# Kernel optimization log

Measured on AMD Instinct MI355X. Metric: run time of the kernel, lower is better.

The kernel has to match this reference:

```python
import jax, jax.numpy as jnp
import numpy as np

BN_EPS = 1e-3  # keras BatchNormalization default epsilon


def _conv(x, w):
    # x: [B,H,W,Cin], w: [kh,kw,Cin,Cout], stride 1, SAME padding
    return jax.lax.conv_general_dilated(
        x, w, window_strides=(1, 1), padding='SAME',
        dimension_numbers=('NHWC', 'HWIO', 'NHWC'))


def _bn(x, g, b, m, v):
    return (x - m) * jax.lax.rsqrt(v + BN_EPS) * g + b


def _pam(x, wq, bq, wk, bk, wv, bv, gamma):
    # Position attention: softmax over HW x HW similarity of 1x1-conv q/k.
    B, H, W, C = x.shape
    q = (_conv(x, wq) + bq).reshape(B, H * W, -1)   # [B,HW,C/8]
    k = (_conv(x, wk) + bk).reshape(B, H * W, -1)   # [B,HW,C/8]
    v = (_conv(x, wv) + bv).reshape(B, H * W, C)    # [B,HW,C]
    energy = jnp.einsum('bic,bjc->bij', q, k)       # [B,HW,HW]
    att = jax.nn.softmax(energy, axis=-1)
    out = jnp.einsum('bij,bjc->bic', att, v).reshape(B, H, W, C)
    return gamma * out + x


def _cam(x, gamma):
    # Channel attention with max-subtract stabilization, softmax over C.
    B, H, W, C = x.shape
    X = x.reshape(B, H * W, C)                      # channel-last flat
    energy = jnp.einsum('bnc,bnd->bcd', X, X)       # [B,C,C]
    energy_new = jnp.max(energy, axis=-1, keepdims=True) - energy
    att = jax.nn.softmax(energy_new, axis=-1)       # [B,C,C]
    out = jnp.einsum('bcd,bnd->bnc', att, X).reshape(B, H, W, C)
    return gamma * out + x


def setup_inputs() -> dict:
    key = jax.random.key(0)
    ks = jax.random.split(key, 16)
    B, H, W = 4, 64, 64
    Cin, Ci, Cq, Cout = 512, 128, 16, 19
    s = 0.05
    d = {
        'x': jax.random.normal(ks[0], (B, H, W, Cin), jnp.float32),
        'w5a': jax.random.normal(ks[1], (3, 3, Cin, Ci), jnp.float32) * s,
        'w5c': jax.random.normal(ks[2], (3, 3, Cin, Ci), jnp.float32) * s,
        'wq': jax.random.normal(ks[3], (1, 1, Ci, Cq), jnp.float32) * s,
        'bq': jnp.zeros((Cq,), jnp.float32),
        'wk': jax.random.normal(ks[4], (1, 1, Ci, Cq), jnp.float32) * s,
        'bk': jnp.zeros((Cq,), jnp.float32),
        'wv': jax.random.normal(ks[5], (1, 1, Ci, Ci), jnp.float32) * s,
        'bv': jnp.zeros((Ci,), jnp.float32),
        'pam_gamma': jnp.float32(0.5),
        'cam_gamma': jnp.float32(0.5),
        'w51': jax.random.normal(ks[6], (3, 3, Ci, Ci), jnp.float32) * s,
        'w52': jax.random.normal(ks[7], (3, 3, Ci, Ci), jnp.float32) * s,
        'w8': jax.random.normal(ks[8], (1, 1, Ci, Cout), jnp.float32) * s,
    }
    for i, nm in enumerate(['bn1', 'bn2', 'bn3', 'bn4']):
        d[nm + '_g'] = jnp.ones((Ci,), jnp.float32)
        d[nm + '_b'] = jnp.zeros((Ci,), jnp.float32)
        d[nm + '_m'] = jax.random.normal(ks[9 + i], (Ci,), jnp.float32) * 0.1
        d[nm + '_v'] = jnp.ones((Ci,), jnp.float32)
    return d


def reference(x, w5a, w5c, wq, bq, wk, bk, wv, bv, pam_gamma, cam_gamma,
              w51, w52, w8,
              bn1_g, bn1_b, bn1_m, bn1_v,
              bn2_g, bn2_b, bn2_m, bn2_v,
              bn3_g, bn3_b, bn3_m, bn3_v,
              bn4_g, bn4_b, bn4_m, bn4_v):
    # PAM branch
    feat1 = jax.nn.relu(_bn(_conv(x, w5a), bn1_g, bn1_b, bn1_m, bn1_v))
    sa_feat = _pam(feat1, wq, bq, wk, bk, wv, bv, pam_gamma)
    sa_conv = jax.nn.relu(_bn(_conv(sa_feat, w51), bn3_g, bn3_b, bn3_m, bn3_v))
    # CAM branch
    feat2 = jax.nn.relu(_bn(_conv(x, w5c), bn2_g, bn2_b, bn2_m, bn2_v))
    sc_feat = _cam(feat2, cam_gamma)
    sc_conv = jax.nn.relu(_bn(_conv(sc_feat, w52), bn4_g, bn4_b, bn4_m, bn4_v))
    # Fused output (dropout is identity at inference)
    feat_sum = sa_conv + sc_conv
    return _conv(feat_sum, w8)
```

## Files before the change

kernel.cpp:

```cpp
#include <hip/hip_runtime.h>
#include <hip/hip_bf16.h>
#include <math.h>

#define BN_EPS 1e-3f
#define LOG2E 1.44269504088896f

constexpr int Bn = 4, Hn = 64, Wn = 64, CIN = 512, CI = 128;
constexpr int HWn = Hn * Wn;
constexpr int NPIX = Bn * HWn;
constexpr int COn = 19;

struct F8 { float4 lo, hi; };

__device__ __forceinline__ F8 f8zero() {
    F8 r; r.lo = make_float4(0.f,0.f,0.f,0.f); r.hi = make_float4(0.f,0.f,0.f,0.f); return r;
}
__device__ __forceinline__ void fma8(F8 &acc, float a, const float4 &wlo, const float4 &whi) {
    acc.lo.x = fmaf(a, wlo.x, acc.lo.x);
    acc.lo.y = fmaf(a, wlo.y, acc.lo.y);
    acc.lo.z = fmaf(a, wlo.z, acc.lo.z);
    acc.lo.w = fmaf(a, wlo.w, acc.lo.w);
    acc.hi.x = fmaf(a, whi.x, acc.hi.x);
    acc.hi.y = fmaf(a, whi.y, acc.hi.y);
    acc.hi.z = fmaf(a, whi.z, acc.hi.z);
    acc.hi.w = fmaf(a, whi.w, acc.hi.w);
}

typedef __attribute__((ext_vector_type(8)))  short    short8;
typedef __attribute__((ext_vector_type(8)))  _Float16 half8;
typedef __attribute__((ext_vector_type(16))) float    f32x16;

__device__ __forceinline__ f32x16 f16z() {
    f32x16 z;
    #pragma unroll
    for (int i = 0; i < 16; ++i) z[i] = 0.f;
    return z;
}
__device__ __forceinline__ unsigned f2b(float f) {
    union { float f; unsigned u; } c; c.f = f;
    return (c.u + 0x7FFFu + ((c.u >> 16) & 1u)) >> 16;
}
__device__ __forceinline__ unsigned pack2(float lo, float hi) {
    return (f2b(hi) << 16) | f2b(lo);
}
__device__ __forceinline__ unsigned pkb2(float a, float b) {
    __hip_bfloat16 ha = __float2bfloat16(a);
    __hip_bfloat16 hb = __float2bfloat16(b);
    return ((unsigned)*(unsigned short*)&hb << 16) | *(unsigned short*)&ha;
}
__device__ __forceinline__ void split2(float a, float b, unsigned &hi, unsigned &lo) {
    const unsigned ha = f2b(a), hb = f2b(b);
    union { unsigned u; float f; } ua, ub; ua.u = ha << 16; ub.u = hb << 16;
    hi = (hb << 16) | ha;
    lo = pack2(a - ua.f, b - ub.f);
}
__device__ __forceinline__ unsigned pkh2(float a, float b) {
    union { _Float16 h; unsigned short u; } ca, cb;
    ca.h = (_Float16)a; cb.h = (_Float16)b;
    return ((unsigned)cb.u << 16) | ca.u;
}

__global__ __launch_bounds__(256)
void k_prep_w(const float* __restrict__ w5a, const float* __restrict__ w5c,
              const float* __restrict__ w51, const float* __restrict__ w52,
              char* __restrict__ wt1F, char* __restrict__ wt2aF, char* __restrict__ wt2bF)
{
    int idx = blockIdx.x * 256 + threadIdx.x;
    if (idx < 589824) {
        const int jp = idx & 7, co = (idx >> 3) & 255, ct = idx >> 11;
        const int tap = ct % 9, c = ct / 9;
        const float* src = (co < 128) ? w5a : w5c;
        const int coc = co & 127;
        const int ci = c*16 + jp*2;
        const float a = src[((size_t)tap*CIN + ci)*CI + coc];
        const float b = src[((size_t)tap*CIN + ci + 1)*CI + coc];
        const int L = co*32 + jp*4;
        *(unsigned*)(wt1F + (size_t)ct*8192 + L) = pkh2(a, b);
    } else {
        int k = idx - 589824;
        if (k >= 147456) return;
        const float* src = (k < 73728) ? w51 : w52;
        char* dstF = (k < 73728) ? wt2aF : wt2bF;
        if (k >= 73728) k -= 73728;
        const int jp = k & 7, co = (k >> 3) & 127, ct = k >> 10;
        const int tap = ct % 9, c = ct / 9;
        const int ci = c*16 + jp*2;
        const float a = src[((size_t)tap*CI + ci)*CI + co];
        const float b = src[((size_t)tap*CI + ci + 1)*CI + co];
        const int L = co*32 + jp*4;
        *(unsigned*)(dstF + (size_t)ct*4096 + L) = pkh2(a, b);
    }
}

__global__ __launch_bounds__(256)
void k_prep_bn(const float* g1, const float* b1, const float* m1, const float* v1,
               const float* g2, const float* b2, const float* m2, const float* v2,
               const float* g3, const float* b3, const float* m3, const float* v3,
               const float* g4, const float* b4, const float* m4, const float* v4,
               float* bnAs, float* bnAb, float* bnBs, float* bnBb)
{
    const int t = threadIdx.x, c = t & 127;
    {
        const float *g = (t < 128) ? g1 : g2, *b = (t < 128) ? b1 : b2;
        const float *m = (t < 128) ? m1 : m2, *v = (t < 128) ? v1 : v2;
        const float s = g[c] * rsqrtf(v[c] + BN_EPS);
        bnAs[t] = s; bnAb[t] = b[c] - m[c]*s;
    }
    {
        const float *g = (t < 128) ? g3 : g4, *b = (t < 128) ? b3 : b4;
        const float *m = (t < 128) ? m3 : m4, *v = (t < 128) ? v3 : v4;
        const float s = g[c] * rsqrtf(v[c] + BN_EPS);
        bnBs[t] = s; bnBb[t] = b[c] - m[c]*s;
    }
}

__global__ __launch_bounds__(256)
void k_prep_x(const float* __restrict__ x, _Float16* __restrict__ xcv)
{
    __shared__ float Xl[16*520];
    const int t = threadIdx.x;
    const int pb = blockIdx.x * 16;
    #pragma unroll
    for (int i = 0; i < 8; ++i) {
        const int u = t + i*256;
        const int px = u >> 7, c4 = (u & 127) * 4;
        *(float4*)&Xl[px*520 + c4] = *(const float4*)&x[(size_t)(pb + px)*CIN + c4];
    }
    __syncthreads();
    const int rowg = pb >> 6, pixb = pb & 63;
    #pragma unroll
    for (int i = 0; i < 8; ++i) {
        const int u = t + i*256;
        const int chunk = u >> 6, rem = u & 63;
        const int pl = rem >> 2, u4 = rem & 3;
        const float* src = &Xl[pl*520 + chunk*16 + u4*4];
        uint2 v;
        v.x = pkh2(src[0], src[1]);
        v.y = pkh2(src[2], src[3]);
        *(uint2*)&xcv[(((size_t)rowg*32 + chunk)*64 + (pixb + pl))*16 + u4*4] = v;
    }
}

template<int NCHNK, int NCOTOT, int WCOBASE>
__global__ __launch_bounds__(256)
void k_convh(const _Float16* __restrict__ xcv0, const _Float16* __restrict__ xcv1,
             const _Float16* __restrict__ wtF0, const _Float16* __restrict__ wtF1,
             const float* __restrict__ bnS, const float* __restrict__ bnBi,
             float* __restrict__ out0, float* __restrict__ out1)
{
    constexpr int XPAGE = 66*32;
    constexpr int XCH   = 3*XPAGE;
    __shared__ __align__(16) char Xs[2*2*XCH];

    const int t    = threadIdx.x;
    const int wgid = blockIdx.x;
    const int xcd  = wgid & 7;
    const int sel  = xcd >> 2;
    const int ch2  = (xcd >> 1) & 1;
    const int row  = ((wgid >> 3) << 1) | (xcd & 1);
    const _Float16* xcv = sel ? xcv1 : xcv0;
    const _Float16* wtF = sel ? wtF1 : wtF0;
    float* dst = sel ? out1 : out0;

    const int hh = row & 63;
    const int dyLo = (hh == 0)  ? 1 : 0;
    const int dyHi = (hh == 63) ? 1 : 2;
    const int l = t & 63, w = t >> 6;
    const int lo5 = l & 31, hf = l >> 5;
    const int mi = w >> 1, nt = w & 1;
    const int corow = WCOBASE*sel + ch2*64 + nt*32 + lo5;

    bool sAct[7], sIn[7]; int sLoff[7]; unsigned sGoff[7];
    #pragma unroll
    for (int i = 0; i < 7; ++i) {
        const int u = t + i*256;
        sAct[i] = false; sIn[i] = false; sLoff[i] = 0; sGoff[i] = 0;
        if (u < 1584) {
            const int cc = (u >= 792) ? 1 : 0;
            const int uu = u - cc*792;
            const int dyr = uu/264, rs = uu - dyr*264;
            const int s = rs >> 2, u4 = rs & 3;
            sAct[i]  = (dyr >= dyLo && dyr <= dyHi);
            sIn[i]   = (s >= 1 && s <= 64);
            sLoff[i] = cc*XCH + dyr*XPAGE + ((s*32 + u4*8) ^ ((s & 7) << 4));
            sGoff[i] = (unsigned)(((row + dyr - 1)*NCHNK + cc)*1024 + (s - 1)*16 + u4*4);
        }
    }
    int xoff[3];
    #pragma unroll
    for (int dx = 0; dx < 3; ++dx) {
        const int s = mi*32 + lo5 + dx;
        xoff[dx] = (s*32 + hf*16) ^ ((s & 7) << 4);
    }

    f32x16 acc = f16z();
    half8 wA[9], wB[9];

    auto issueW9 = [&](int c, half8 (&wr)[9]) {
        #pragma unroll
        for (int tap = 0; tap < 9; ++tap)
            wr[tap] = *(const half8*)&wtF[((size_t)(c*9 + tap)*NCOTOT + corow)*16 + hf*8];
    };
    auto compC = [&](const char* Xb, int cc, const half8 (&wr)[9]) {
        #pragma unroll
        for (int dy = 0; dy < 3; ++dy) {
            if (dy < dyLo || dy > dyHi) continue;
            const char* Xp = Xb + cc*XCH + dy*XPAGE;
            #pragma unroll
            for (int dx = 0; dx < 3; ++dx) {
                const half8 xf = *(const half8*)(Xp + xoff[dx]);
                acc = __builtin_amdgcn_mfma_f32_32x32x16_f16(wr[dy*3 + dx], xf, acc, 0, 0, 0);
            }
        }
    };

    uint2 xr[7];
    auto loadX = [&](int cbase) {
        #pragma unroll
        for (int i = 0; i < 7; ++i) {
            uint2 v; v.x = 0u; v.y = 0u;
            if (sAct[i] && sIn[i])
                v = *(const uint2*)&xcv[(size_t)sGoff[i] + (size_t)cbase*1024];
            xr[i] = v;
        }
    };

    loadX(0);
    int p = 0;
    for (int c = 0; c < NCHNK; c += 2) {
        issueW9(c, wA);
        char* Xb = Xs + p*2*XCH;
        #pragma unroll
        for (int i = 0; i < 7; ++i)
            if (sAct[i]) *(uint2*)(Xb + sLoff[i]) = xr[i];
        __syncthreads();
        if (c + 2 < NCHNK) loadX(c + 2);
        issueW9(c + 1, wB);
        compC(Xb, 0, wA);
        compC(Xb, 1, wB);
        p ^= 1;
    }
    const int px = mi*32 + lo5;
    const size_t pg = (size_t)row*Wn + px;
    #pragma unroll
    for (int r = 0; r < 16; ++r) {
        const int crow = (r & 3) + 8*(r >> 2) + 4*hf;
        const int och = ch2*64 + nt*32 + crow;
        const int bnidx = sel*128 + och;
        dst[pg*CI + och] = fmaxf(fmaf(acc[r], bnS[bnidx], bnBi[bnidx]), 0.f);
    }
}

__global__ __launch_bounds__(256)
void k_qk(const float* __restrict__ feat1,
          const float* __restrict__ wq, const float* __restrict__ bq,
          const float* __restrict__ wk, const float* __restrict__ bk,
          __hip_bfloat16* __restrict__ qb, __hip_bfloat16* __restrict__ kb)
{
    __shared__ float Al[64*129];
    __shared__ __align__(16) float Wl[128*32];
    const int t = threadIdx.x;
    const int pb = blockIdx.x * 64;
    for (int idx = t; idx < 64*128; idx += 256) {
        const int p = idx >> 7, ci = idx & 127;
        Al[p*129 + ci] = feat1[(size_t)(pb + p)*CI + ci];
    }
    for (int idx = t; idx < 128*32; idx += 256) {
        const int ci = idx >> 5, c = idx & 31;
        Wl[idx] = (c < 16) ? wq[ci*16 + c] : wk[ci*16 + (c - 16)];
    }
    __syncthreads();
    const int p = t & 63, cg = t >> 6, co = cg * 8;
    F8 acc = f8zero();
    #pragma unroll 8
    for (int ci = 0; ci < 128; ++ci) {
        const float a = Al[p*129 + ci];
        const float4 wlo = *(const float4*)&Wl[ci*32 + co];
        const float4 whi = *(const float4*)&Wl[ci*32 + co + 4];
        fma8(acc, a, wlo, whi);
    }
    const float* af = (const float*)&acc;
    #pragma unroll
    for (int j = 0; j < 8; ++j) {
        const int c = co + j;
        if (c < 16) qb[(size_t)(pb + p)*16 + c]        = __float2bfloat16((af[j] + bq[c]) * LOG2E);
        else        kb[(size_t)(pb + p)*16 + (c - 16)] = __float2bfloat16(af[j] + bk[c - 16]);
    }
}

__global__ __launch_bounds__(256)
void k_v(const float* __restrict__ feat1, const float* __restrict__ wv,
         const float* __restrict__ bv, __hip_bfloat16* __restrict__ vbT)
{
    __shared__ float Al[32*129];
    __shared__ __align__(16) float Wl[64*128];
    const int t = threadIdx.x;
    const int pb = blockIdx.x * 32;
    for (int idx = t; idx < 32*128; idx += 256) {
        const int p = idx >> 7, ci = idx & 127;
        Al[p*129 + ci] = feat1[(size_t)(pb + p)*CI + ci];
    }
    const int px = t & 15, co = (t >> 4) * 8;
    F8 acc0 = f8zero(), acc1 = f8zero();
    for (int ch = 0; ch < 2; ++ch) {
        __syncthreads();
        #pragma unroll
        for (int r = 0; r < 8; ++r) {
            const int i4 = t + r*256;
            const int kk = i4 >> 5, c4 = (i4 & 31) * 4;
            *(float4*)&Wl[kk*128 + c4] = *(const float4*)&wv[(size_t)(ch*64 + kk)*CI + c4];
        }
        __syncthreads();
        #pragma unroll 4
        for (int kk = 0; kk < 64; ++kk) {
            const float a0 = Al[px*129 + ch*64 + kk];
            const float a1 = Al[(px+16)*129 + ch*64 + kk];
            const float4 wlo = *(const float4*)&Wl[kk*128 + co];
            const float4 whi = *(const float4*)&Wl[kk*128 + co + 4];
            fma8(acc0, a0, wlo, whi);
            fma8(acc1, a1, wlo, whi);
        }
    }
    const int p0 = pb + px;
    const int bb = p0 / HWn, pin0 = p0 % HWn;
    const int k16a = pin0 >> 4, ko = pin0 & 15;
    const float* a0f = (const float*)&acc0;
    const float* a1f = (const float*)&acc1;
    #pragma unroll
    for (int j = 0; j < 8; ++j) {
        const int c = co + j;
        const size_t base = ((size_t)bb*256*CI*16) + (size_t)c*16 + ko;
        vbT[base + (size_t)k16a*CI*16]       = __float2bfloat16(a0f[j] + bv[c]);
        vbT[base + (size_t)(k16a + 1)*CI*16] = __float2bfloat16(a1f[j] + bv[c]);
    }
}

__global__ __launch_bounds__(256)
void k_pam(const __hip_bfloat16* __restrict__ qb, const __hip_bfloat16* __restrict__ kb,
           const __hip_bfloat16* __restrict__ vbT, const float* __restrict__ feat1,
           const float* __restrict__ gamma, _Float16* __restrict__ saf_h)
{
    __shared__ __align__(16) char pbuf[16896];
    __shared__ float msArr[4][32];
    __shared__ float ssArr[4][32];
    __shared__ float ssum[32];
    const int t  = threadIdx.x;
    const int wv = t >> 6, l = t & 63;
    const int lo5 = l & 31, h = l >> 5;
    unsigned* Ppk = (unsigned*)(pbuf + wv*4096);
    float* osum = (float*)pbuf;

    const int q0 = blockIdx.x * 32;
    const int bb = q0 / HWn;
    const size_t jb = (size_t)bb * HWn;
    const __hip_bfloat16* vbB = vbT + (size_t)bb * 256 * CI * 16;

    const short8 qfrag = *(const short8*)&qb[(size_t)(q0 + lo5)*16 + 8*h];
    const f32x16 zro = f16z();

    f32x16 o[4];
    #pragma unroll
    for (int cb = 0; cb < 4; ++cb) o[cb] = f16z();

    float m_run = -1e30f, s_run = 0.f;

    for (int k0 = wv*1024; k0 < wv*1024 + 1024; k0 += 64) {
        const short8 kf0 = *(const short8*)&kb[(jb + k0 +      lo5)*16 + 8*h];
        const short8 kf1 = *(const short8*)&kb[(jb + k0 + 32 + lo5)*16 + 8*h];
        short8 vf[4][4];
        #pragma unroll
        for (int s = 0; s < 4; ++s)
            #pragma unroll
            for (int cb = 0; cb < 4; ++cb)
                vf[s][cb] = *(const short8*)&vbB[
                    (((size_t)(k0 >> 4) + s)*CI + cb*32 + lo5)*16 + 8*h];

        f32x16 e0 = __builtin_amdgcn_mfma_f32_32x32x16_bf16(kf0, qfrag, zro, 0, 0, 0);
        f32x16 e1 = __builtin_amdgcn_mfma_f32_32x32x16_bf16(kf1, qfrag, zro, 0, 0, 0);

        float mt = fmaxf(e0[0], e1[0]);
        #pragma unroll
        for (int r = 1; r < 16; ++r) mt = fmaxf(mt, fmaxf(e0[r], e1[r]));
        mt = fmaxf(mt, __shfl_xor(mt, 32));

        if (__any(mt > m_run + 11.5416f)) {
            const float mnew = fmaxf(m_run, mt);
            const float sc = exp2f(m_run - mnew);
            s_run *= sc;
            #pragma unroll
            for (int cb = 0; cb < 4; ++cb)
                #pragma unroll
                for (int r = 0; r < 16; ++r) o[cb][r] *= sc;
            m_run = mnew;
        }

        #pragma unroll
        for (int r = 0; r < 16; ++r) {
            e0[r] = exp2f(e0[r] - m_run);
            e1[r] = exp2f(e1[r] - m_run);
        }
        float ss = 0.f;
        #pragma unroll
        for (int r = 0; r < 16; ++r) ss += e0[r] + e1[r];
        s_run += ss;

        #pragma unroll
        for (int r = 0; r < 16; r += 2) {
            const int pidx = ((r & 3) >> 1) + 4*(r >> 2) + 2*h;
            Ppk[pidx*32 + lo5]        = pkb2(e0[r], e0[r+1]);
            Ppk[(16 + pidx)*32 + lo5] = pkb2(e1[r], e1[r+1]);
        }
        #pragma unroll
        for (int s = 0; s < 4; ++s) {
            union { unsigned u[4]; short8 s8; } P;
            #pragma unroll
            for (int w = 0; w < 4; ++w)
                P.u[w] = Ppk[(s*8 + 4*h + w)*32 + lo5];
            #pragma unroll
            for (int cb = 0; cb < 4; ++cb)
                o[cb] = __builtin_amdgcn_mfma_f32_32x32x16_bf16(vf[s][cb], P.s8, o[cb], 0, 0, 0);
        }
    }

    const float s_w = s_run + __shfl_xor(s_run, 32);
    if (h == 0) { msArr[wv][lo5] = m_run; ssArr[wv][lo5] = s_w; }
    __syncthreads();

    float M = msArr[0][lo5];
    #pragma unroll
    for (int w = 1; w < 4; ++w) M = fmaxf(M, msArr[w][lo5]);
    float stot = 0.f;
    #pragma unroll
    for (int w = 0; w < 4; ++w) stot += exp2f(msArr[w][lo5] - M) * ssArr[w][lo5];
    if (wv == 0 && h == 0) ssum[lo5] = stot;
    const float myscale = exp2f(m_run - M);
    #pragma unroll
    for (int cb = 0; cb < 4; ++cb)
        #pragma unroll
        for (int r = 0; r < 16; ++r) o[cb][r] *= myscale;

    for (int w = 0; w < 4; ++w) {
        if (wv == w) {
            #pragma unroll
            for (int cb = 0; cb < 4; ++cb)
                #pragma unroll
                for (int r = 0; r < 16; ++r) {
                    const int c = cb*32 + (r & 3) + 8*(r >> 2) + 4*h;
                    float* p = &osum[lo5*132 + c];
                    if (w == 0) *p = o[cb][r]; else *p += o[cb][r];
                }
        }
        __syncthreads();
    }

    const float g = gamma[0];
    const int qloc = t >> 3, ch8 = t & 7;
    const float inv = 1.f / ssum[qloc];
    const int pgl = q0 + qloc;
    const int rowp = pgl >> 6, pixp = pgl & 63;
    const size_t gbase = (size_t)pgl*CI + ch8*16;
    union { _Float16 hv[16]; uint4 u[2]; } tmp;
    #pragma unroll
    for (int j = 0; j < 16; ++j)
        tmp.hv[j] = (_Float16)(g*(osum[qloc*132 + ch8*16 + j]*inv) + feat1[gbase + j]);
    uint4* dsth = (uint4*)&saf_h[((size_t)(rowp*8 + ch8)*64 + pixp)*16];
    dsth[0] = tmp.u[0];
    dsth[1] = tmp.u[1];
}

__global__ __launch_bounds__(256)
void k_xpose(const float* __restrict__ feat2,
             char* __restrict__ f2TH, char* __restrict__ f2TL)
{
    __shared__ float Xl[64*129];
    const int t = threadIdx.x;
    const int pb = blockIdx.x * 64;
    const int bb = pb / HWn, pin = pb % HWn;
    for (int idx = t; idx < 64*128; idx += 256) {
        const int p = idx >> 7, ci = idx & 127;
        Xl[p*129 + ci] = feat2[(size_t)(pb + p)*CI + ci];
    }
    __syncthreads();
    const int c = t >> 1, half = t & 1;
    const size_t rowb = ((size_t)(bb*CI + c)*HWn + pin + half*32) * 2;
    #pragma unroll
    for (int j = 0; j < 16; ++j) {
        const float a = Xl[(half*32 + 2*j)*129 + c];
        const float b = Xl[(half*32 + 2*j + 1)*129 + c];
        unsigned hi, lo; split2(a, b, hi, lo);
        *(unsigned*)(f2TH + rowb + 4*j) = hi;
        *(unsigned*)(f2TL + rowb + 4*j) = lo;
    }
}

__global__ __launch_bounds__(256)
void k_cam_energy_m(const char* __restrict__ f2TH, const char* __restrict__ f2TL,
                    float* __restrict__ epart)
{
    __shared__ __align__(16) char Vh[128*256];
    __shared__ __align__(16) char Vl[128*256];
    const int t = threadIdx.x;
    const int ks = blockIdx.x, bb = blockIdx.y;
    const int l = t & 63, w = t >> 6;
    const int lo5 = l & 31, hf = l >> 5;

    #pragma unroll
    for (int pass = 0; pass < 8; ++pass) {
        const int slot = pass*256 + t;
        const int c = slot >> 4, g = slot & 15;
        const size_t gaddr = ((size_t)(bb*CI + c)*HWn + ks*128)*2 + g*16;
        const int laddr = c*256 + ((g*16) ^ ((c & 15) << 4));
        *(float4*)(Vh + laddr) = *(const float4*)(f2TH + gaddr);
        *(float4*)(Vl + laddr) = *(const float4*)(f2TL + gaddr);
    }
    __syncthreads();

    f32x16 acc[4];
    #pragma unroll
    for (int nj = 0; nj < 4; ++nj) acc[nj] = f16z();
    const int cA = w*32 + lo5;
    const int swA = (cA & 15) << 4;

    #pragma unroll
    for (int kk = 0; kk < 8; ++kk) {
        const int kb = kk*32 + hf*16;
        const short8 ah = *(const short8*)(Vh + cA*256 + (kb ^ swA));
        const short8 al = *(const short8*)(Vl + cA*256 + (kb ^ swA));
        #pragma unroll
        for (int nj = 0; nj < 4; ++nj) {
            const int dB = nj*32 + lo5;
            const int swB = (dB & 15) << 4;
            const short8 bh = *(const short8*)(Vh + dB*256 + (kb ^ swB));
            const short8 bl = *(const short8*)(Vl + dB*256 + (kb ^ swB));
            acc[nj] = __builtin_amdgcn_mfma_f32_32x32x16_bf16(ah, bh, acc[nj], 0, 0, 0);
            acc[nj] = __builtin_amdgcn_mfma_f32_32x32x16_bf16(al, bh, acc[nj], 0, 0, 0);
            acc[nj] = __builtin_amdgcn_mfma_f32_32x32x16_bf16(ah, bl, acc[nj], 0, 0, 0);
        }
    }
    float* ep = epart + ((size_t)(bb*32 + ks)*CI)*CI;
    #pragma unroll
    for (int nj = 0; nj < 4; ++nj)
        #pragma unroll
        for (int r = 0; r < 16; ++r) {
            const int c = w*32 + (r & 3) + 8*(r >> 2) + 4*hf;
            ep[(size_t)c*CI + nj*32 + lo5] = acc[nj][r];
        }
}

__global__ __launch_bounds__(64)
void k_cam_rs(const float* __restrict__ epart, float* __restrict__ att)
{
    const int lane = threadIdx.x;
    const int row = blockIdx.x;
    const int bb = row >> 7, c = row & 127;
    float2 e = make_float2(0.f, 0.f);
    for (int ks = 0; ks < 32; ++ks) {
        const float2 v = *(const float2*)&epart[
            ((size_t)(bb*32 + ks)*CI + c)*CI + lane*2];
        e.x += v.x; e.y += v.y;
    }
    float M = fmaxf(e.x, e.y);
    #pragma unroll
    for (int off = 32; off > 0; off >>= 1) M = fmaxf(M, __shfl_xor(M, off));
    const float en0 = M - e.x, en1 = M - e.y;
    float mx = fmaxf(en0, en1);
    #pragma unroll
    for (int off = 32; off > 0; off >>= 1) mx = fmaxf(mx, __shfl_xor(mx, off));
    const float p0 = __expf(en0 - mx), p1 = __expf(en1 - mx);
    float s = p0 + p1;
    #pragma unroll
    for (int off = 32; off > 0; off >>= 1) s += __shfl_xor(s, off);
    const float inv = 1.f / s;
    float2 o; o.x = p0*inv; o.y = p1*inv;
    *(float2*)&att[(size_t)row*CI + lane*2] = o;
}

__global__ __launch_bounds__(256)
void k_cam_apply(const float* __restrict__ feat2, const float* __restrict__ att,
                 const float* __restrict__ gamma, _Float16* __restrict__ scf_h)
{
    __shared__ float Xl[64*129];
    __shared__ __align__(16) float aT[128*64];
    const int t = threadIdx.x;
    const int pb = blockIdx.x * 64;
    const int bb = pb / HWn;
    const int ch = blockIdx.y * 64;
    for (int idx = t; idx < 64*128; idx += 256) {
        const int p = idx >> 7, ci = idx & 127;
        Xl[p*129 + ci] = feat2[(size_t)(pb + p)*CI + ci];
    }
    for (int idx = t; idx < 128*64; idx += 256) {
        const int d = idx >> 6, cc = idx & 63;
        aT[d*64 + cc] = att[((size_t)bb*CI + ch + cc)*CI + d];
    }
    __syncthreads();
    const int px = t & 63, cg = t >> 6;
    F8 accA = f8zero(), accB = f8zero();
    #pragma unroll 4
    for (int d = 0; d < 128; ++d) {
        const float xv = Xl[px*129 + d];
        const float* ap = &aT[d*64 + cg*16];
        const float4 a0 = *(const float4*)&ap[0];
        const float4 a1 = *(const float4*)&ap[4];
        const float4 a2 = *(const float4*)&ap[8];
        const float4 a3 = *(const float4*)&ap[12];
        fma8(accA, xv, a0, a1);
        fma8(accB, xv, a2, a3);
    }
    const float g = gamma[0];
    const float* fa = (const float*)&accA;
    const float* fb = (const float*)&accB;
    const int p0g = pb + px;
    const int rowA = p0g >> 6, pixA = p0g & 63;
    const int chunkA = (ch >> 4) + cg;
    const size_t baseA = ((size_t)(rowA*8 + chunkA)*64 + pixA)*16;
    #pragma unroll
    for (int j = 0; j < 8; ++j) {
        const int cA = ch + cg*16 + j;
        const int cB = cA + 8;
        scf_h[baseA + j]     = (_Float16)(g*fa[j] + Xl[px*129 + cA]);
        scf_h[baseA + 8 + j] = (_Float16)(g*fb[j] + Xl[px*129 + cB]);
    }
}

__global__ __launch_bounds__(256)
void k_final(const float* __restrict__ sa, const float* __restrict__ sc,
             const float* __restrict__ w8, float* __restrict__ out)
{
    __shared__ float Xl[64*129];
    __shared__ float w8l[128*COn];
    const int t = threadIdx.x;
    const int pb = blockIdx.x * 64;
    for (int idx = t; idx < 64*128; idx += 256) {
        const int p = idx >> 7, ci = idx & 127;
        const size_t gi = (size_t)(pb + p)*CI + ci;
        Xl[p*129 + ci] = sa[gi] + sc[gi];
    }
    for (int idx = t; idx < 128*COn; idx += 256) w8l[idx] = w8[idx];
    __syncthreads();
    for (int idx = t; idx < 64*COn; idx += 256) {
        const int p = idx / COn, co = idx - p*COn;
        float acc = 0.f;
        #pragma unroll 8
        for (int ci = 0; ci < 128; ++ci)
            acc = fmaf(Xl[p*129 + ci], w8l[ci*COn + co], acc);
        out[(size_t)(pb + p)*COn + co] = acc;
    }
}

extern "C" void kernel_launch(void* const* d_in, const int* in_sizes, int n_in,
                              void* d_out, int out_size, void* d_ws, size_t ws_size,
                              hipStream_t stream)
{
    const float* x    = (const float*)d_in[0];
    const float* w5a  = (const float*)d_in[1];
    const float* w5c  = (const float*)d_in[2];
    const float* wq   = (const float*)d_in[3];
    const float* bq   = (const float*)d_in[4];
    const float* wk   = (const float*)d_in[5];
    const float* bk   = (const float*)d_in[6];
    const float* wv   = (const float*)d_in[7];
    const float* bv   = (const float*)d_in[8];
    const float* pgam = (const float*)d_in[9];
    const float* cgam = (const float*)d_in[10];
    const float* w51  = (const float*)d_in[11];
    const float* w52  = (const float*)d_in[12];
    const float* w8   = (const float*)d_in[13];
    const float* bn1g = (const float*)d_in[14];
    const float* bn1b = (const float*)d_in[15];
    const float* bn1m = (const float*)d_in[16];
    const float* bn1v = (const float*)d_in[17];
    const float* bn2g = (const float*)d_in[18];
    const float* bn2b = (const float*)d_in[19];
    const float* bn2m = (const float*)d_in[20];
    const float* bn2v = (const float*)d_in[21];
    const float* bn3g = (const float*)d_in[22];
    const float* bn3b = (const float*)d_in[23];
    const float* bn3m = (const float*)d_in[24];
    const float* bn3v = (const float*)d_in[25];
    const float* bn4g = (const float*)d_in[26];
    const float* bn4b = (const float*)d_in[27];
    const float* bn4m = (const float*)d_in[28];
    const float* bn4v = (const float*)d_in[29];

    char* wsb = (char*)d_ws;
    float* feat1 = (float*)(wsb + 0);
    char*  f2TH  = wsb + 0;
    char*  f2TL  = wsb + 4194304;
    float* feat2 = (float*)(wsb + 8388608);
    _Float16* xcv   = (_Float16*)(wsb + 16777216);
    _Float16* saf_h = (_Float16*)(wsb + 16777216);
    _Float16* scf_h = (_Float16*)(wsb + 20971520);
    float*    epart = (float*)(wsb + 25165824);
    float* att = (float*)(wsb + 33816576);
    __hip_bfloat16* qb16 = (__hip_bfloat16*)(wsb + 34078720);
    __hip_bfloat16* kb16 = (__hip_bfloat16*)(wsb + 34603008);
    __hip_bfloat16* vbT  = (__hip_bfloat16*)(wsb + 35127296);
    char* wt1F  = wsb + 39321600;
    char* wt2aF = wsb + 41680896;
    char* wt2bF = wsb + 41975808;
    float* bnAs = (float*)(wsb + 42270720);
    float* bnAb = (float*)(wsb + 42271744);
    float* bnBs = (float*)(wsb + 42272768);
    float* bnBb = (float*)(wsb + 42273792);
    float* sa_conv = feat1;
    float* sc_conv = feat2;
    float* out  = (float*)d_out;

    k_prep_w<<<dim3(2880), 256, 0, stream>>>(w5a, w5c, w51, w52, wt1F, wt2aF, wt2bF);
    k_prep_bn<<<dim3(1), 256, 0, stream>>>(bn1g, bn1b, bn1m, bn1v, bn2g, bn2b, bn2m, bn2v,
                                           bn3g, bn3b, bn3m, bn3v, bn4g, bn4b, bn4m, bn4v,
                                           bnAs, bnAb, bnBs, bnBb);
    k_prep_x<<<dim3(1024), 256, 0, stream>>>(x, xcv);
    k_convh<32, 256, 128><<<dim3(1024), 256, 0, stream>>>(
        xcv, xcv, (const _Float16*)wt1F, (const _Float16*)wt1F, bnAs, bnAb, feat1, feat2);
    k_qk<<<dim3(NPIX/64), 256, 0, stream>>>(feat1, wq, bq, wk, bk, qb16, kb16);
    k_v<<<dim3(NPIX/32), 256, 0, stream>>>(feat1, wv, bv, vbT);
    k_pam<<<dim3(NPIX/32), 256, 0, stream>>>(qb16, kb16, vbT, feat1, pgam, saf_h);
    k_xpose<<<dim3(NPIX/64), 256, 0, stream>>>(feat2, f2TH, f2TL);
    k_cam_energy_m<<<dim3(32, Bn), 256, 0, stream>>>(f2TH, f2TL, epart);
    k_cam_rs<<<dim3(Bn*CI), 64, 0, stream>>>(epart, att);
    k_cam_apply<<<dim3(NPIX/64, 2), 256, 0, stream>>>(feat2, att, cgam, scf_h);
    k_convh<8, 128, 0><<<dim3(1024), 256, 0, stream>>>(
        saf_h, scf_h, (const _Float16*)wt2aF, (const _Float16*)wt2bF,
        bnBs, bnBb, sa_conv, sc_conv);
    k_final<<<dim3(NPIX/64), 256, 0, stream>>>(sa_conv, sc_conv, w8, out);
}
```

Baseline: 232.0 us.

## Read conv inputs directly from halo-padded global layout instead of LDS staging

The fp16 conv inputs (xcv, saf_h, scf_h) get a padded layout with a zeroed one-pixel halo on each side of every row. A new k_zhalo kernel zeroes the halo slots for the second-stage buffers, and k_prep_x zeroes them for the first. The 3x3 conv kernel drops its double-buffered LDS tile, the barriers and the boundary predicates. Each MFMA operand, input and weight, is now loaded straight from global memory per channel chunk. This removes LDS traffic and synchronisation but relies on L1/L2 to absorb the threefold overlapping reads across dx, and leaves less software prefetch to hide latency.

```diff
diff --git a/kernel.cpp b/kernel.cpp
--- a/kernel.cpp
+++ b/kernel.cpp
@@ -9,6 +9,8 @@
 constexpr int HWn = Hn * Wn;
 constexpr int NPIX = Bn * HWn;
 constexpr int COn = 19;
+constexpr int XSL = 66;
+constexpr int XPG = XSL * 16;
 
 struct F8 { float4 lo, hi; };
 
@@ -137,21 +139,36 @@
         uint2 v;
         v.x = pkh2(src[0], src[1]);
         v.y = pkh2(src[2], src[3]);
-        *(uint2*)&xcv[(((size_t)rowg*32 + chunk)*64 + (pixb + pl))*16 + u4*4] = v;
-    }
+        *(uint2*)&xcv[(((size_t)rowg*32 + chunk)*XSL + (pixb + pl + 1))*16 + u4*4] = v;
+    }
+    if (pixb == 0 && t < 64) {
+        const int chunk = t >> 1, sl = (t & 1) * 65;
+        uint4* dst = (uint4*)&xcv[(((size_t)rowg*32 + chunk)*XSL + sl)*16];
+        uint4 z; z.x = 0u; z.y = 0u; z.z = 0u; z.w = 0u;
+        dst[0] = z; dst[1] = z;
+    }
+}
+
+__global__ __launch_bounds__(256)
+void k_zhalo(_Float16* __restrict__ saf_h, _Float16* __restrict__ scf_h)
+{
+    const int idx = blockIdx.x * 256 + threadIdx.x;
+    if (idx >= 8192) return;
+    _Float16* arr = (idx & 4096) ? scf_h : saf_h;
+    const int rem = idx & 4095;
+    const int row = rem >> 4, chunk = (rem >> 1) & 7, sl = (rem & 1) * 65;
+    uint4* dst = (uint4*)&arr[(((size_t)row*8 + chunk)*XSL + sl)*16];
+    uint4 z; z.x = 0u; z.y = 0u; z.z = 0u; z.w = 0u;
+    dst[0] = z; dst[1] = z;
 }
 
 template<int NCHNK, int NCOTOT, int WCOBASE>
 __global__ __launch_bounds__(256)
-void k_convh(const _Float16* __restrict__ xcv0, const _Float16* __restrict__ xcv1,
+void k_convg(const _Float16* __restrict__ xcv0, const _Float16* __restrict__ xcv1,
              const _Float16* __restrict__ wtF0, const _Float16* __restrict__ wtF1,
              const float* __restrict__ bnS, const float* __restrict__ bnBi,
              float* __restrict__ out0, float* __restrict__ out1)
 {
-    constexpr int XPAGE = 66*32;
-    constexpr int XCH   = 3*XPAGE;
-    __shared__ __align__(16) char Xs[2*2*XCH];
-
     const int t    = threadIdx.x;
     const int wgid = blockIdx.x;
     const int xcd  = wgid & 7;
@@ -170,75 +187,29 @@
     const int mi = w >> 1, nt = w & 1;
     const int corow = WCOBASE*sel + ch2*64 + nt*32 + lo5;
 
-    bool sAct[7], sIn[7]; int sLoff[7]; unsigned sGoff[7];
-    #pragma unroll
-    for (int i = 0; i < 7; ++i) {
-        const int u = t + i*256;
-        sAct[i] = false; sIn[i] = false; sLoff[i] = 0; sGoff[i] = 0;
-        if (u < 1584) {
-            const int cc = (u >= 792) ? 1 : 0;
-            const int uu = u - cc*792;
-            const int dyr = uu/264, rs = uu - dyr*264;
-            const int s = rs >> 2, u4 = rs & 3;
-            sAct[i]  = (dyr >= dyLo && dyr <= dyHi);
-            sIn[i]   = (s >= 1 && s <= 64);
-            sLoff[i] = cc*XCH + dyr*XPAGE + ((s*32 + u4*8) ^ ((s & 7) << 4));
-            sGoff[i] = (unsigned)(((row + dyr - 1)*NCHNK + cc)*1024 + (s - 1)*16 + u4*4);
-        }
-    }
-    int xoff[3];
-    #pragma unroll
-    for (int dx = 0; dx < 3; ++dx) {
-        const int s = mi*32 + lo5 + dx;
-        xoff[dx] = (s*32 + hf*16) ^ ((s & 7) << 4);
-    }
+    unsigned xbase[3];
+    #pragma unroll
+    for (int dy = 0; dy < 3; ++dy)
+        xbase[dy] = (unsigned)(((row + dy - 1)*NCHNK)*XPG + (mi*32 + lo5)*16 + hf*8);
+    const unsigned wbase = (unsigned)(corow*16 + hf*8);
 
     f32x16 acc = f16z();
-    half8 wA[9], wB[9];
-
-    auto issueW9 = [&](int c, half8 (&wr)[9]) {
-        #pragma unroll
-        for (int tap = 0; tap < 9; ++tap)
-            wr[tap] = *(const half8*)&wtF[((size_t)(c*9 + tap)*NCOTOT + corow)*16 + hf*8];
-    };
-    auto compC = [&](const char* Xb, int cc, const half8 (&wr)[9]) {
+
+    #pragma unroll 2
+    for (int c = 0; c < NCHNK; ++c) {
         #pragma unroll
         for (int dy = 0; dy < 3; ++dy) {
             if (dy < dyLo || dy > dyHi) continue;
-            const char* Xp = Xb + cc*XCH + dy*XPAGE;
+            half8 wf[3], xf[3];
             #pragma unroll
             for (int dx = 0; dx < 3; ++dx) {
-                const half8 xf = *(const half8*)(Xp + xoff[dx]);
-                acc = __builtin_amdgcn_mfma_f32_32x32x16_f16(wr[dy*3 + dx], xf, acc, 0, 0, 0);
+                wf[dx] = *(const half8*)&wtF[(size_t)((c*9 + dy*3 + dx)*NCOTOT)*16 + wbase];
+                xf[dx] = *(const half8*)&xcv[(size_t)xbase[dy] + (size_t)c*XPG + dx*16];
             }
-        }
-    };
-
-    uint2 xr[7];
-    auto loadX = [&](int cbase) {
-        #pragma unroll
-        for (int i = 0; i < 7; ++i) {
-            uint2 v; v.x = 0u; v.y = 0u;
-            if (sAct[i] && sIn[i])
-                v = *(const uint2*)&xcv[(size_t)sGoff[i] + (size_t)cbase*1024];
-            xr[i] = v;
-        }
-    };
-
-    loadX(0);
-    int p = 0;
-    for (int c = 0; c < NCHNK; c += 2) {
-        issueW9(c, wA);
-        char* Xb = Xs + p*2*XCH;
-        #pragma unroll
-        for (int i = 0; i < 7; ++i)
-            if (sAct[i]) *(uint2*)(Xb + sLoff[i]) = xr[i];
-        __syncthreads();
-        if (c + 2 < NCHNK) loadX(c + 2);
-        issueW9(c + 1, wB);
-        compC(Xb, 0, wA);
-        compC(Xb, 1, wB);
-        p ^= 1;
+            #pragma unroll
+            for (int dx = 0; dx < 3; ++dx)
+                acc = __builtin_amdgcn_mfma_f32_32x32x16_f16(wf[dx], xf[dx], acc, 0, 0, 0);
+        }
     }
     const int px = mi*32 + lo5;
     const size_t pg = (size_t)row*Wn + px;
@@ -463,7 +434,7 @@
     #pragma unroll
     for (int j = 0; j < 16; ++j)
         tmp.hv[j] = (_Float16)(g*(osum[qloc*132 + ch8*16 + j]*inv) + feat1[gbase + j]);
-    uint4* dsth = (uint4*)&saf_h[((size_t)(rowp*8 + ch8)*64 + pixp)*16];
+    uint4* dsth = (uint4*)&saf_h[(((size_t)rowp*8 + ch8)*XSL + (pixp + 1))*16];
     dsth[0] = tmp.u[0];
     dsth[1] = tmp.u[1];
 }
@@ -613,7 +584,7 @@
     const int p0g = pb + px;
     const int rowA = p0g >> 6, pixA = p0g & 63;
     const int chunkA = (ch >> 4) + cg;
-    const size_t baseA = ((size_t)(rowA*8 + chunkA)*64 + pixA)*16;
+    const size_t baseA = (((size_t)rowA*8 + chunkA)*XSL + (pixA + 1))*16;
     #pragma unroll
     for (int j = 0; j < 8; ++j) {
         const int cA = ch + cg*16 + j;
@@ -690,8 +661,8 @@
     float* feat2 = (float*)(wsb + 8388608);
     _Float16* xcv   = (_Float16*)(wsb + 16777216);
     _Float16* saf_h = (_Float16*)(wsb + 16777216);
-    _Float16* scf_h = (_Float16*)(wsb + 20971520);
-    float*    epart = (float*)(wsb + 25165824);
+    _Float16* scf_h = (_Float16*)(wsb + 21102592);
+    float*    epart = (float*)(wsb + 25427968);
     float* att = (float*)(wsb + 33816576);
     __hip_bfloat16* qb16 = (__hip_bfloat16*)(wsb + 34078720);
     __hip_bfloat16* kb16 = (__hip_bfloat16*)(wsb + 34603008);
@@ -712,8 +683,9 @@
                                            bn3g, bn3b, bn3m, bn3v, bn4g, bn4b, bn4m, bn4v,
                                            bnAs, bnAb, bnBs, bnBb);
     k_prep_x<<<dim3(1024), 256, 0, stream>>>(x, xcv);
-    k_convh<32, 256, 128><<<dim3(1024), 256, 0, stream>>>(
+    k_convg<32, 256, 128><<<dim3(1024), 256, 0, stream>>>(
         xcv, xcv, (const _Float16*)wt1F, (const _Float16*)wt1F, bnAs, bnAb, feat1, feat2);
+    k_zhalo<<<dim3(32), 256, 0, stream>>>(saf_h, scf_h);
     k_qk<<<dim3(NPIX/64), 256, 0, stream>>>(feat1, wq, bq, wk, bk, qb16, kb16);
     k_v<<<dim3(NPIX/32), 256, 0, stream>>>(feat1, wv, bv, vbT);
     k_pam<<<dim3(NPIX/32), 256, 0, stream>>>(qb16, kb16, vbT, feat1, pgam, saf_h);
@@ -721,7 +693,7 @@
     k_cam_energy_m<<<dim3(32, Bn), 256, 0, stream>>>(f2TH, f2TL, epart);
     k_cam_rs<<<dim3(Bn*CI), 64, 0, stream>>>(epart, att);
     k_cam_apply<<<dim3(NPIX/64, 2), 256, 0, stream>>>(feat2, att, cgam, scf_h);
-    k_convh<8, 128, 0><<<dim3(1024), 256, 0, stream>>>(
+    k_convg<8, 128, 0><<<dim3(1024), 256, 0, stream>>>(
         saf_h, scf_h, (const _Float16*)wt2aF, (const _Float16*)wt2bF,
         bnBs, bnBb, sa_conv, sc_conv);
     k_final<<<dim3(NPIX/64), 256, 0, stream>>>(sa_conv, sc_conv, w8, out);
```

Measured after the change: 243.3 us. 1.05x slower.
